# Kernel tuning notes

Hardware: AMD Instinct MI355X
Metric: run time of the kernel (lower is better)

## Reference

```python
import jax, jax.numpy as jnp
import numpy as np

REG = 0.1      # ot_reg (entropic regularization)
TAU = 0.5      # ot_tau (marginal relaxation reg_m)
N_ITERS = 100  # fixed iteration count (POT default numItermax=1000 with early stop)


def setup_inputs() -> dict:
    key = jax.random.key(0)
    kx, ky = jax.random.split(key)
    x = jax.random.normal(kx, (8192, 1, 512), dtype=jnp.float32)
    y = jax.random.normal(ky, (4096, 1, 512), dtype=jnp.float32)
    return {"x": x, "y": y}


def _normalize_feature(x):
    # x - x.min(-1, keepdim)  (shift each row to be non-negative-min)
    return x - jnp.min(x, axis=-1, keepdims=True)


def reference(x, y):
    # x: (N,1,D), y: (M,1,D)
    x = _normalize_feature(x[:, 0, :])  # (N,D)
    y = _normalize_feature(y[:, 0, :])  # (M,D)

    # squared euclidean cost: cdist(x,y)**2, via gram trick (N,M)
    x2 = jnp.sum(x * x, axis=1)[:, None]
    y2 = jnp.sum(y * y, axis=1)[None, :]
    cost = jnp.maximum(x2 + y2 - 2.0 * (x @ y.T), 0.0)

    # normalized, detached cost used for the OT solve
    Mn = jax.lax.stop_gradient(cost / jnp.max(cost))
    K = jnp.exp(-Mn / REG)  # (N,M) Gibbs kernel

    n, m = K.shape
    a = 1.0 / n  # uniform source marginal (scalar since all entries equal)
    b = 1.0 / m  # uniform target marginal
    fi = TAU / (TAU + REG)

    u0 = jnp.full((n,), 1.0 / n, dtype=K.dtype)
    v0 = jnp.full((m,), 1.0 / m, dtype=K.dtype)

    def step(carry, _):
        u, v = carry
        u = (a / (K @ v)) ** fi       # (N,)
        v = (b / (K.T @ u)) ** fi     # (M,)
        return (u, v), None

    (u, v), _ = jax.lax.scan(step, (u0, v0), None, length=N_ITERS)

    flow = u[:, None] * K * v[None, :]          # (N,M), detached w.r.t. cost
    dist = jnp.sum(cost * flow)                  # scalar, grads flow via cost

    pi = flow.T[None, None, :, :]                # (1,1,M,N)
    return pi, dist
```

## Files before the change

kernel.cpp:

```cpp
#include <hip/hip_runtime.h>

#define N_ROWS 8192
#define M_ROWS 4096
#define D_DIM  512
#define N_ITERS 100
constexpr size_t NM = (size_t)N_ROWS * (size_t)M_ROWS;
constexpr float FREG   = 0.1f;
constexpr float FI     = 0.5f / (0.5f + 0.1f);
constexpr float A_MARG = 1.0f / (float)N_ROWS;
constexpr float B_MARG = 1.0f / (float)M_ROWS;
#define FIN_BLOCKS 16384

__device__ __forceinline__ unsigned short f2bf(float f) {
    unsigned int u = __float_as_uint(f);
    u += 0x7fffu + ((u >> 16) & 1u);
    return (unsigned short)(u >> 16);
}
__device__ __forceinline__ float bflo(unsigned int u) { return __uint_as_float(u << 16); }
__device__ __forceinline__ float bfhi(unsigned int u) { return __uint_as_float(u & 0xffff0000u); }
__device__ __forceinline__ unsigned int pack2(float a, float b) {
    return (unsigned int)f2bf(a) | ((unsigned int)f2bf(b) << 16);
}

__global__ void __launch_bounds__(256) init_kernel(float* v, unsigned int* maxc) {
    int t = blockIdx.x * 256 + threadIdx.x;
    if (t < M_ROWS) v[t] = B_MARG;
    if (t == 0) *maxc = 0u;
}

__global__ void __launch_bounds__(256) rownorm_kernel(const float* __restrict__ x,
                                                      unsigned short* __restrict__ xn,
                                                      float* __restrict__ x2) {
    int lane = threadIdx.x & 63;
    int row  = blockIdx.x * 4 + (threadIdx.x >> 6);
    const float* p = x + (size_t)row * D_DIM + lane * 8;
    float4 v0 = *(const float4*)p;
    float4 v1 = *(const float4*)(p + 4);
    float a[8] = {v0.x, v0.y, v0.z, v0.w, v1.x, v1.y, v1.z, v1.w};
    float mn = a[0];
#pragma unroll
    for (int t = 1; t < 8; ++t) mn = fminf(mn, a[t]);
#pragma unroll
    for (int o = 32; o >= 1; o >>= 1) mn = fminf(mn, __shfl_xor(mn, o, 64));
    float ss = 0.0f;
#pragma unroll
    for (int t = 0; t < 8; ++t) { a[t] -= mn; ss = fmaf(a[t], a[t], ss); }
#pragma unroll
    for (int o = 32; o >= 1; o >>= 1) ss += __shfl_xor(ss, o, 64);
    uint4 pk;
    pk.x = pack2(a[0], a[1]); pk.y = pack2(a[2], a[3]);
    pk.z = pack2(a[4], a[5]); pk.w = pack2(a[6], a[7]);
    *(uint4*)(xn + (size_t)row * D_DIM + lane * 8) = pk;
    if (lane == 0) x2[row] = ss;
}

typedef __attribute__((ext_vector_type(8))) short short8;
typedef __attribute__((ext_vector_type(4))) float f32x4;

__global__ void __launch_bounds__(256) gemm_cost_kernel(const unsigned short* __restrict__ xn,
                                                        const unsigned short* __restrict__ yn,
                                                        const float* __restrict__ x2,
                                                        const float* __restrict__ y2,
                                                        unsigned short* __restrict__ cost,
                                                        unsigned int* __restrict__ maxc) {
    __shared__ unsigned short As[128 * 40];
    __shared__ unsigned short Bs[128 * 40];
    __shared__ float wred[4];
    int tid = threadIdx.x, lane = tid & 63, w = tid >> 6;
    int wm = w >> 1, wn = w & 1;
    int i0 = blockIdx.x * 128, j0 = blockIdx.y * 128;
    int lr = tid >> 2;
    int lq = tid & 3;
    f32x4 acc[4][4] = {};
    int m = lane & 15, quad = lane >> 4;

    for (int k0 = 0; k0 < D_DIM; k0 += 32) {
        uint4 a0 = *(const uint4*)(xn + (size_t)(i0 + lr) * D_DIM + k0 + lq * 8);
        uint4 a1 = *(const uint4*)(xn + (size_t)(i0 + lr + 64) * D_DIM + k0 + lq * 8);
        uint4 b0 = *(const uint4*)(yn + (size_t)(j0 + lr) * D_DIM + k0 + lq * 8);
        uint4 b1 = *(const uint4*)(yn + (size_t)(j0 + lr + 64) * D_DIM + k0 + lq * 8);
        __syncthreads();
        *(uint4*)&As[lr * 40 + lq * 8]        = a0;
        *(uint4*)&As[(lr + 64) * 40 + lq * 8] = a1;
        *(uint4*)&Bs[lr * 40 + lq * 8]        = b0;
        *(uint4*)&Bs[(lr + 64) * 40 + lq * 8] = b1;
        __syncthreads();
        short8 af[4], bfr[4];
#pragma unroll
        for (int t = 0; t < 4; ++t) {
            af[t]  = *(const short8*)&As[(wm * 64 + t * 16 + m) * 40 + quad * 8];
            bfr[t] = *(const short8*)&Bs[(wn * 64 + t * 16 + m) * 40 + quad * 8];
        }
#pragma unroll
        for (int tm = 0; tm < 4; ++tm)
#pragma unroll
            for (int tn = 0; tn < 4; ++tn)
                acc[tm][tn] = __builtin_amdgcn_mfma_f32_16x16x32_bf16(af[tm], bfr[tn], acc[tm][tn], 0, 0, 0);
    }

    float mymax = 0.0f;
#pragma unroll
    for (int tm = 0; tm < 4; ++tm) {
#pragma unroll
        for (int tn = 0; tn < 4; ++tn) {
            int col = j0 + wn * 64 + tn * 16 + m;
            float yv = y2[col];
#pragma unroll
            for (int t = 0; t < 4; ++t) {
                int row = i0 + wm * 64 + tm * 16 + quad * 4 + t;
                float c = fmaxf(x2[row] + yv - 2.0f * acc[tm][tn][t], 0.0f);
                mymax = fmaxf(mymax, c);
                cost[(size_t)row * M_ROWS + col] = f2bf(c);
            }
        }
    }
#pragma unroll
    for (int o = 32; o >= 1; o >>= 1) mymax = fmaxf(mymax, __shfl_xor(mymax, o, 64));
    if (lane == 0) wred[w] = mymax;
    __syncthreads();
    if (tid == 0) {
        float mx = fmaxf(fmaxf(wred[0], wred[1]), fmaxf(wred[2], wred[3]));
        atomicMax(maxc, __float_as_uint(mx));
    }
}

__global__ void __launch_bounds__(256) expT_kernel(unsigned short* __restrict__ Kmat,
                                                   unsigned short* __restrict__ KTmat,
                                                   const unsigned int* __restrict__ maxcb) {
    __shared__ unsigned int tl[64 * 33];
    float scale = -(1.0f / FREG) / __uint_as_float(*maxcb);
    int i0 = blockIdx.x * 64, j0 = blockIdx.y * 64;
    int tid = threadIdx.x;
    int b = tid & 7;
    int rp = tid >> 3;
    size_t base0 = (size_t)(i0 + 2 * rp) * M_ROWS + j0 + b * 8;
    uint4 c0 = *(const uint4*)(Kmat + base0);
    uint4 c1 = *(const uint4*)(Kmat + base0 + M_ROWS);
    unsigned int cc0[4] = {c0.x, c0.y, c0.z, c0.w};
    unsigned int cc1[4] = {c1.x, c1.y, c1.z, c1.w};
    float k0[8], k1[8];
#pragma unroll
    for (int t = 0; t < 4; ++t) {
        k0[2 * t]     = expf(bflo(cc0[t]) * scale);
        k0[2 * t + 1] = expf(bfhi(cc0[t]) * scale);
        k1[2 * t]     = expf(bflo(cc1[t]) * scale);
        k1[2 * t + 1] = expf(bfhi(cc1[t]) * scale);
    }
    uint4 o0, o1;
    o0.x = pack2(k0[0], k0[1]); o0.y = pack2(k0[2], k0[3]);
    o0.z = pack2(k0[4], k0[5]); o0.w = pack2(k0[6], k0[7]);
    o1.x = pack2(k1[0], k1[1]); o1.y = pack2(k1[2], k1[3]);
    o1.z = pack2(k1[4], k1[5]); o1.w = pack2(k1[6], k1[7]);
    *(uint4*)(Kmat + base0)          = o0;
    *(uint4*)(Kmat + base0 + M_ROWS) = o1;
#pragma unroll
    for (int t = 0; t < 8; ++t)
        tl[(b * 8 + t) * 33 + rp] = pack2(k0[t], k1[t]);
    __syncthreads();
    int c = tid >> 2, q = tid & 3;
    unsigned int o[8];
#pragma unroll
    for (int k = 0; k < 8; ++k) o[k] = tl[c * 33 + q * 8 + k];
    uint4 w0 = {o[0], o[1], o[2], o[3]};
    uint4 w1 = {o[4], o[5], o[6], o[7]};
    size_t ob = (size_t)(j0 + c) * N_ROWS + i0 + q * 16;
    *(uint4*)(KTmat + ob)     = w0;
    *(uint4*)(KTmat + ob + 8) = w1;
}

__global__ void __launch_bounds__(256) u_step_kernel(const unsigned short* __restrict__ Km,
                                                     const float* __restrict__ v,
                                                     float* __restrict__ u) {
    int tid = threadIdx.x, lane = tid & 63, w = tid >> 6;
    int r = blockIdx.x * 4 + w;
    const unsigned short* kp = Km + (size_t)r * M_ROWS + lane * 8;
    const float* vp = v + lane * 8;
    float a0 = 0.0f, a1 = 0.0f, a2 = 0.0f, a3 = 0.0f;
#pragma unroll
    for (int s = 0; s < 8; ++s) {
        uint4 kk = *(const uint4*)(kp + s * 512);
        float4 v0 = *(const float4*)(vp + s * 512);
        float4 v1 = *(const float4*)(vp + s * 512 + 4);
        a0 = fmaf(bflo(kk.x), v0.x, a0);
        a1 = fmaf(bfhi(kk.x), v0.y, a1);
        a2 = fmaf(bflo(kk.y), v0.z, a2);
        a3 = fmaf(bfhi(kk.y), v0.w, a3);
        a0 = fmaf(bflo(kk.z), v1.x, a0);
        a1 = fmaf(bfhi(kk.z), v1.y, a1);
        a2 = fmaf(bflo(kk.w), v1.z, a2);
        a3 = fmaf(bfhi(kk.w), v1.w, a3);
    }
    float dot = (a0 + a1) + (a2 + a3);
#pragma unroll
    for (int o = 32; o >= 1; o >>= 1) dot += __shfl_xor(dot, o, 64);
    if (lane == 0) u[r] = powf(A_MARG / dot, FI);
}

__global__ void __launch_bounds__(256) v_step_kernel(const unsigned short* __restrict__ KTm,
                                                     const float* __restrict__ u,
                                                     float* __restrict__ v) {
    int tid = threadIdx.x, lane = tid & 63, w = tid >> 6;
    int r = blockIdx.x * 4 + w;
    const unsigned short* kp = KTm + (size_t)r * N_ROWS + lane * 8;
    const float* up = u + lane * 8;
    float a0 = 0.0f, a1 = 0.0f, a2 = 0.0f, a3 = 0.0f;
#pragma unroll
    for (int s = 0; s < 16; ++s) {
        uint4 kk = *(const uint4*)(kp + s * 512);
        float4 v0 = *(const float4*)(up + s * 512);
        float4 v1 = *(const float4*)(up + s * 512 + 4);
        a0 = fmaf(bflo(kk.x), v0.x, a0);
        a1 = fmaf(bfhi(kk.x), v0.y, a1);
        a2 = fmaf(bflo(kk.y), v0.z, a2);
        a3 = fmaf(bfhi(kk.y), v0.w, a3);
        a0 = fmaf(bflo(kk.z), v1.x, a0);
        a1 = fmaf(bfhi(kk.z), v1.y, a1);
        a2 = fmaf(bflo(kk.w), v1.z, a2);
        a3 = fmaf(bfhi(kk.w), v1.w, a3);
    }
    float dot = (a0 + a1) + (a2 + a3);
#pragma unroll
    for (int o = 32; o >= 1; o >>= 1) dot += __shfl_xor(dot, o, 64);
    if (lane == 0) v[r] = powf(B_MARG / dot, FI);
}

__global__ void __launch_bounds__(256) finalize_kernel(const unsigned short* __restrict__ KTm,
                                                       const float* __restrict__ u,
                                                       const float* __restrict__ v,
                                                       const unsigned int* __restrict__ maxcb,
                                                       float* __restrict__ out,
                                                       float* __restrict__ part) {
    __shared__ float red[4];
    int tid = threadIdx.x, lane = tid & 63;
    size_t base = ((size_t)blockIdx.x * 256 + tid) * 8;
    int mrow = (int)(base >> 13);
    int n    = (int)(base & 8191);
    float cscale = -FREG * __uint_as_float(*maxcb);
    uint4 kk = *(const uint4*)(KTm + base);
    float4 u0 = *(const float4*)(u + n);
    float4 u1 = *(const float4*)(u + n + 4);
    float vm = v[mrow];
    float kv[8] = {bflo(kk.x), bfhi(kk.x), bflo(kk.y), bfhi(kk.y),
                   bflo(kk.z), bfhi(kk.z), bflo(kk.w), bfhi(kk.w)};
    float uu[8] = {u0.x, u0.y, u0.z, u0.w, u1.x, u1.y, u1.z, u1.w};
    float fl[8];
    float ds = 0.0f;
#pragma unroll
    for (int t = 0; t < 8; ++t) {
        fl[t] = uu[t] * kv[t] * vm;
        ds = fmaf(cscale * logf(kv[t]), fl[t], ds);
    }
    float4 w0 = {fl[0], fl[1], fl[2], fl[3]};
    float4 w1 = {fl[4], fl[5], fl[6], fl[7]};
    *(float4*)(out + base)     = w0;
    *(float4*)(out + base + 4) = w1;
#pragma unroll
    for (int o = 32; o >= 1; o >>= 1) ds += __shfl_xor(ds, o, 64);
    if (lane == 0) red[tid >> 6] = ds;
    __syncthreads();
    if (tid == 0) part[blockIdx.x] = red[0] + red[1] + red[2] + red[3];
}

__global__ void __launch_bounds__(256) reduce_dist_kernel(const float* __restrict__ part,
                                                          float* __restrict__ dist) {
    __shared__ float red[4];
    int tid = threadIdx.x, lane = tid & 63;
    float s = 0.0f;
    for (int i = tid; i < FIN_BLOCKS; i += 256) s += part[i];
#pragma unroll
    for (int o = 32; o >= 1; o >>= 1) s += __shfl_xor(s, o, 64);
    if (lane == 0) red[tid >> 6] = s;
    __syncthreads();
    if (tid == 0) *dist = red[0] + red[1] + red[2] + red[3];
}

extern "C" void kernel_launch(void* const* d_in, const int* in_sizes, int n_in,
                              void* d_out, int out_size, void* d_ws, size_t ws_size,
                              hipStream_t stream) {
    const float* x = (const float*)d_in[0];
    const float* y = (const float*)d_in[1];
    float* out = (float*)d_out;
    char* ws = (char*)d_ws;

    unsigned short* Kmat = (unsigned short*)(ws);
    unsigned short* KT   = (unsigned short*)(ws + 67108864);
    unsigned short* xn   = (unsigned short*)(ws + 134217728);
    unsigned short* yn   = (unsigned short*)(ws + 142606336);
    float* x2            = (float*)(ws + 146800640);
    float* y2            = (float*)(ws + 146833408);
    float* u             = (float*)(ws + 146849792);
    float* v             = (float*)(ws + 146882560);
    unsigned int* maxc   = (unsigned int*)(ws + 146898944);
    float* part          = (float*)(ws + 134217728);
    float* dist = out + NM;

    init_kernel<<<16, 256, 0, stream>>>(v, maxc);
    rownorm_kernel<<<N_ROWS / 4, 256, 0, stream>>>(x, xn, x2);
    rownorm_kernel<<<M_ROWS / 4, 256, 0, stream>>>(y, yn, y2);
    gemm_cost_kernel<<<dim3(N_ROWS / 128, M_ROWS / 128), 256, 0, stream>>>(xn, yn, x2, y2, Kmat, maxc);
    expT_kernel<<<dim3(N_ROWS / 64, M_ROWS / 64), 256, 0, stream>>>(Kmat, KT, maxc);

    for (int it = 0; it < N_ITERS; ++it) {
        u_step_kernel<<<N_ROWS / 4, 256, 0, stream>>>(Kmat, v, u);
        v_step_kernel<<<M_ROWS / 4, 256, 0, stream>>>(KT, u, v);
    }

    finalize_kernel<<<FIN_BLOCKS, 256, 0, stream>>>(KT, u, v, maxc, out, part);
    reduce_dist_kernel<<<1, 256, 0, stream>>>(part, dist);
}
```

Measured before the change: 2.750 ms.

## Pipeline Sinkhorn matvecs with async global-to-LDS loads and multi-row waves

Rewrites the u and v Sinkhorn matvec kernels so each wave handles several rows (4 for u, 2 for v) and reuses the v/u vector held in registers across them. The K tiles are double-buffered through LDS using global_load_lds async copies, with explicit vmcnt waits so the next tile is in flight while the current one is consumed. Grid sizes drop to 512 blocks per step. The goal is more memory-level parallelism on the bandwidth-bound matvecs over the bf16 K matrices. The cost is heavier register use and fewer blocks, which may reduce occupancy.

```diff
diff --git a/kernel.cpp b/kernel.cpp
--- a/kernel.cpp
+++ b/kernel.cpp
@@ -21,6 +21,18 @@
 __device__ __forceinline__ unsigned int pack2(float a, float b) {
     return (unsigned int)f2bf(a) | ((unsigned int)f2bf(b) << 16);
 }
+
+typedef __attribute__((address_space(1))) void gvoid;
+typedef __attribute__((address_space(3))) void lvoid;
+__device__ __forceinline__ void async_load16(const void* g, void* l) {
+    __builtin_amdgcn_global_load_lds((gvoid*)g, (lvoid*)l, 16, 0, 0);
+}
+
+#define FMA8(ac, kk, A, B)                                          \
+    ac = fmaf(bflo(kk.x), A.x, ac); ac = fmaf(bfhi(kk.x), A.y, ac); \
+    ac = fmaf(bflo(kk.y), A.z, ac); ac = fmaf(bfhi(kk.y), A.w, ac); \
+    ac = fmaf(bflo(kk.z), B.x, ac); ac = fmaf(bfhi(kk.z), B.y, ac); \
+    ac = fmaf(bflo(kk.w), B.z, ac); ac = fmaf(bfhi(kk.w), B.w, ac);
 
 __global__ void __launch_bounds__(256) init_kernel(float* v, unsigned int* maxc) {
     int t = blockIdx.x * 256 + threadIdx.x;
@@ -168,60 +180,100 @@
     *(uint4*)(KTmat + ob + 8) = w1;
 }
 
-__global__ void __launch_bounds__(256) u_step_kernel(const unsigned short* __restrict__ Km,
-                                                     const float* __restrict__ v,
-                                                     float* __restrict__ u) {
+__global__ void __launch_bounds__(256, 2) u_step_kernel(const unsigned short* __restrict__ Km,
+                                                        const float* __restrict__ v,
+                                                        float* __restrict__ u) {
+    __shared__ __align__(16) char buf[4][2][4096];
     int tid = threadIdx.x, lane = tid & 63, w = tid >> 6;
-    int r = blockIdx.x * 4 + w;
-    const unsigned short* kp = Km + (size_t)r * M_ROWS + lane * 8;
-    const float* vp = v + lane * 8;
-    float a0 = 0.0f, a1 = 0.0f, a2 = 0.0f, a3 = 0.0f;
+    int r0 = blockIdx.x * 16 + w * 4;
+    float4 va[8], vb[8];
+    const float4* vp = (const float4*)v;
 #pragma unroll
     for (int s = 0; s < 8; ++s) {
-        uint4 kk = *(const uint4*)(kp + s * 512);
-        float4 v0 = *(const float4*)(vp + s * 512);
-        float4 v1 = *(const float4*)(vp + s * 512 + 4);
-        a0 = fmaf(bflo(kk.x), v0.x, a0);
-        a1 = fmaf(bfhi(kk.x), v0.y, a1);
-        a2 = fmaf(bflo(kk.y), v0.z, a2);
-        a3 = fmaf(bfhi(kk.y), v0.w, a3);
-        a0 = fmaf(bflo(kk.z), v1.x, a0);
-        a1 = fmaf(bfhi(kk.z), v1.y, a1);
-        a2 = fmaf(bflo(kk.w), v1.z, a2);
-        a3 = fmaf(bfhi(kk.w), v1.w, a3);
-    }
-    float dot = (a0 + a1) + (a2 + a3);
-#pragma unroll
-    for (int o = 32; o >= 1; o >>= 1) dot += __shfl_xor(dot, o, 64);
-    if (lane == 0) u[r] = powf(A_MARG / dot, FI);
-}
-
-__global__ void __launch_bounds__(256) v_step_kernel(const unsigned short* __restrict__ KTm,
-                                                     const float* __restrict__ u,
-                                                     float* __restrict__ v) {
+        va[s] = vp[s * 128 + lane * 2];
+        vb[s] = vp[s * 128 + lane * 2 + 1];
+    }
+    char* wbuf = &buf[w][0][0];
+    const unsigned short* kbase = Km + (size_t)r0 * M_ROWS + lane * 8;
+    float acc[4] = {0.0f, 0.0f, 0.0f, 0.0f};
+
+#define STAGE_U(ss) {                                              \
+        const unsigned short* sp = kbase + (ss) * 512;             \
+        char* dst = wbuf + ((ss) & 1) * 4096;                      \
+        async_load16(sp,              dst);                        \
+        async_load16(sp +     M_ROWS, dst + 1024);                 \
+        async_load16(sp + 2 * M_ROWS, dst + 2048);                 \
+        async_load16(sp + 3 * M_ROWS, dst + 3072); }
+
+    STAGE_U(0);
+#pragma unroll
+    for (int s = 0; s < 8; ++s) {
+        if (s < 7) { STAGE_U(s + 1); asm volatile("s_waitcnt vmcnt(4)" ::: "memory"); }
+        else       { asm volatile("s_waitcnt vmcnt(0)" ::: "memory"); }
+        const char* src = wbuf + (s & 1) * 4096 + lane * 16;
+        uint4 k0 = *(const uint4*)(src);
+        uint4 k1 = *(const uint4*)(src + 1024);
+        uint4 k2 = *(const uint4*)(src + 2048);
+        uint4 k3 = *(const uint4*)(src + 3072);
+        float4 A = va[s], B = vb[s];
+        FMA8(acc[0], k0, A, B);
+        FMA8(acc[1], k1, A, B);
+        FMA8(acc[2], k2, A, B);
+        FMA8(acc[3], k3, A, B);
+    }
+#undef STAGE_U
+#pragma unroll
+    for (int i = 0; i < 4; ++i) {
+        float d = acc[i];
+#pragma unroll
+        for (int o = 32; o >= 1; o >>= 1) d += __shfl_xor(d, o, 64);
+        if (lane == 0) u[r0 + i] = powf(A_MARG / d, FI);
+    }
+}
+
+__global__ void __launch_bounds__(256, 1) v_step_kernel(const unsigned short* __restrict__ KTm,
+                                                        const float* __restrict__ u,
+                                                        float* __restrict__ vout) {
+    __shared__ __align__(16) char buf[4][2][2048];
     int tid = threadIdx.x, lane = tid & 63, w = tid >> 6;
-    int r = blockIdx.x * 4 + w;
-    const unsigned short* kp = KTm + (size_t)r * N_ROWS + lane * 8;
-    const float* up = u + lane * 8;
-    float a0 = 0.0f, a1 = 0.0f, a2 = 0.0f, a3 = 0.0f;
+    int r0 = blockIdx.x * 8 + w * 2;
+    float4 ua[16], ub[16];
+    const float4* up = (const float4*)u;
 #pragma unroll
     for (int s = 0; s < 16; ++s) {
-        uint4 kk = *(const uint4*)(kp + s * 512);
-        float4 v0 = *(const float4*)(up + s * 512);
-        float4 v1 = *(const float4*)(up + s * 512 + 4);
-        a0 = fmaf(bflo(kk.x), v0.x, a0);
-        a1 = fmaf(bfhi(kk.x), v0.y, a1);
-        a2 = fmaf(bflo(kk.y), v0.z, a2);
-        a3 = fmaf(bfhi(kk.y), v0.w, a3);
-        a0 = fmaf(bflo(kk.z), v1.x, a0);
-        a1 = fmaf(bfhi(kk.z), v1.y, a1);
-        a2 = fmaf(bflo(kk.w), v1.z, a2);
-        a3 = fmaf(bfhi(kk.w), v1.w, a3);
-    }
-    float dot = (a0 + a1) + (a2 + a3);
-#pragma unroll
-    for (int o = 32; o >= 1; o >>= 1) dot += __shfl_xor(dot, o, 64);
-    if (lane == 0) v[r] = powf(B_MARG / dot, FI);
+        ua[s] = up[s * 128 + lane * 2];
+        ub[s] = up[s * 128 + lane * 2 + 1];
+    }
+    char* wbuf = &buf[w][0][0];
+    const unsigned short* kbase = KTm + (size_t)r0 * N_ROWS + lane * 8;
+    float acc[2] = {0.0f, 0.0f};
+
+#define STAGE_V(ss) {                                              \
+        const unsigned short* sp = kbase + (ss) * 512;             \
+        char* dst = wbuf + ((ss) & 1) * 2048;                      \
+        async_load16(sp,          dst);                            \
+        async_load16(sp + N_ROWS, dst + 1024); }
+
+    STAGE_V(0);
+#pragma unroll
+    for (int s = 0; s < 16; ++s) {
+        if (s < 15) { STAGE_V(s + 1); asm volatile("s_waitcnt vmcnt(2)" ::: "memory"); }
+        else        { asm volatile("s_waitcnt vmcnt(0)" ::: "memory"); }
+        const char* src = wbuf + (s & 1) * 2048 + lane * 16;
+        uint4 k0 = *(const uint4*)(src);
+        uint4 k1 = *(const uint4*)(src + 1024);
+        float4 A = ua[s], B = ub[s];
+        FMA8(acc[0], k0, A, B);
+        FMA8(acc[1], k1, A, B);
+    }
+#undef STAGE_V
+#pragma unroll
+    for (int i = 0; i < 2; ++i) {
+        float d = acc[i];
+#pragma unroll
+        for (int o = 32; o >= 1; o >>= 1) d += __shfl_xor(d, o, 64);
+        if (lane == 0) vout[r0 + i] = powf(B_MARG / d, FI);
+    }
 }
 
 __global__ void __launch_bounds__(256) finalize_kernel(const unsigned short* __restrict__ KTm,
@@ -301,8 +353,8 @@
     expT_kernel<<<dim3(N_ROWS / 64, M_ROWS / 64), 256, 0, stream>>>(Kmat, KT, maxc);
 
     for (int it = 0; it < N_ITERS; ++it) {
-        u_step_kernel<<<N_ROWS / 4, 256, 0, stream>>>(Kmat, v, u);
-        v_step_kernel<<<M_ROWS / 4, 256, 0, stream>>>(KT, u, v);
+        u_step_kernel<<<512, 256, 0, stream>>>(Kmat, v, u);
+        v_step_kernel<<<512, 256, 0, stream>>>(KT, u, v);
     }
 
     finalize_kernel<<<FIN_BLOCKS, 256, 0, stream>>>(KT, u, v, maxc, out, part);
```

Result: slower. 3.633 ms (+32.1%).
